# Performance work log

Measured on AMD Instinct MI355X. Metric: run time of the kernel, lower is better.

The kernel has to match this reference:

```python
import jax, jax.numpy as jnp
import numpy as np

B, N, C, H = 4, 2048, 1024, 16
D = C // H

def setup_inputs() -> dict:
    key = jax.random.key(0)
    k1, k2, k3 = jax.random.split(key, 3)
    x = jax.random.normal(k1, (B, N, C), dtype=jnp.float32)
    w_qkv = jax.random.normal(k2, (C, 3 * C), dtype=jnp.float32) * (C ** -0.5)
    w_proj = jax.random.normal(k3, (C, C), dtype=jnp.float32) * (C ** -0.5)
    b_proj = jnp.zeros((C,), dtype=jnp.float32)
    return {"x": x, "w_qkv": w_qkv, "w_proj": w_proj, "b_proj": b_proj}

def reference(x, w_qkv, w_proj, b_proj):
    scale = D ** -0.5
    qkv = x @ w_qkv                                   # [B,N,3C]
    qkv = qkv.reshape(B, N, 3, H, D).transpose(2, 0, 3, 1, 4)  # [3,B,H,N,D]
    q, k, v = qkv[0], qkv[1], qkv[2]
    attn = jnp.einsum('bhnd,bhmd->bhnm', q, k) * scale  # [B,H,N,N]
    attn = jax.nn.softmax(attn, axis=-1)
    o = jnp.einsum('bhnm,bhmd->bhnd', attn, v)          # [B,H,N,D]
    o = o.transpose(0, 2, 1, 3).reshape(B, N, C)
    return o @ w_proj + b_proj
```

## Files before the change

### kernel.cpp

```cpp
#include <hip/hip_runtime.h>
#include <hip/hip_bf16.h>


#define B_ 4
#define N_ 2048
#define C_ 1024
#define H_ 16
#define D_ 64
#define MCONST 24.0f

typedef __attribute__((ext_vector_type(8))) __bf16 bf16x8;
typedef __attribute__((ext_vector_type(4))) float f32x4;
typedef __attribute__((ext_vector_type(16))) float f32x16;
typedef unsigned int u32;
typedef __attribute__((ext_vector_type(2))) u32 u32x2;
typedef __attribute__((ext_vector_type(4))) u32 u32x4;

__device__ inline unsigned short f2bf(float f) {
  __bf16 h = (__bf16)f;
  return __builtin_bit_cast(unsigned short, h);
}

__device__ __forceinline__ u32 pk2(float lo, float hi) {
  return (u32)f2bf(lo) | ((u32)f2bf(hi) << 16);
}

__device__ __forceinline__ void gld16(const void* g, void* l) {
  __builtin_amdgcn_global_load_lds(
      (const __attribute__((address_space(1))) u32*)g,
      (__attribute__((address_space(3))) u32*)l, 16, 0, 0);
}

__global__ __launch_bounds__(256) void cvt_bf16_kernel(
    const float* __restrict__ in, unsigned short* __restrict__ out) {
  int i = (blockIdx.x * 256 + threadIdx.x) * 8;
  float4 f0 = *(const float4*)&in[i];
  float4 f1 = *(const float4*)&in[i + 4];
  ushort4 h0, h1;
  h0.x = f2bf(f0.x); h0.y = f2bf(f0.y); h0.z = f2bf(f0.z); h0.w = f2bf(f0.w);
  h1.x = f2bf(f1.x); h1.y = f2bf(f1.y); h1.z = f2bf(f1.z); h1.w = f2bf(f1.w);
  *(ushort4*)&out[i] = h0;
  *(ushort4*)&out[i + 4] = h1;
}

__global__ __launch_bounds__(256) void transpose_cvt_kernel(
    const float* __restrict__ in, unsigned short* __restrict__ out,
    int K, int Nn) {
  __shared__ float tile[32][33];
  const int t = threadIdx.x;
  const int k0 = blockIdx.y * 32, n0 = blockIdx.x * 32;
  {
    int r = t >> 3, c = (t & 7) * 4;
    float4 f = *(const float4*)&in[(size_t)(k0 + r) * Nn + n0 + c];
    tile[r][c + 0] = f.x; tile[r][c + 1] = f.y;
    tile[r][c + 2] = f.z; tile[r][c + 3] = f.w;
  }
  __syncthreads();
  {
    int nr = t >> 3, kc = (t & 7) * 4;
    ushort4 h;
    h.x = f2bf(tile[kc + 0][nr]);
    h.y = f2bf(tile[kc + 1][nr]);
    h.z = f2bf(tile[kc + 2][nr]);
    h.w = f2bf(tile[kc + 3][nr]);
    *(ushort4*)&out[(size_t)(n0 + nr) * K + k0 + kc] = h;
  }
}

__global__ __launch_bounds__(256) void transpose_v_kernel(
    const unsigned short* __restrict__ vb, unsigned short* __restrict__ vtb) {
  __shared__ u32 tile[64][65];
  const int tid = threadIdx.x;
  const int n0 = blockIdx.x * 64;
  const int bh = blockIdx.y;
  const size_t base = (size_t)bh * N_ * D_;
#pragma unroll
  for (int i = 0; i < 2; i++) {
    int id = i * 256 + tid;
    int row = id >> 3, c8 = id & 7;
    uint4 v = *(const uint4*)&vb[base + (size_t)(n0 + row) * D_ + c8 * 8];
    const unsigned short* pv = (const unsigned short*)&v;
#pragma unroll
    for (int j = 0; j < 8; j++) tile[row][c8 * 8 + j] = pv[j];
  }
  __syncthreads();
#pragma unroll
  for (int i = 0; i < 2; i++) {
    int id = i * 256 + tid;
    int d = id >> 3, nc = id & 7;
    uint4 o;
    unsigned short* po = (unsigned short*)&o;
#pragma unroll
    for (int j = 0; j < 8; j++) po[j] = (unsigned short)tile[nc * 8 + j][d];
    *(uint4*)&vtb[base + (size_t)d * N_ + n0 + nc * 8] = o;
  }
}

template<int MODE>
__global__ __launch_bounds__(256) void gemm128_kernel(
    const unsigned short* __restrict__ A, const unsigned short* __restrict__ Bt,
    const float* __restrict__ bias,
    unsigned short* __restrict__ qb, unsigned short* __restrict__ kb,
    unsigned short* __restrict__ vb, float* __restrict__ outp,
    int M, int K, int Nout)
{
  __shared__ unsigned short Al[128 * 64];
  __shared__ unsigned short Bl[128 * 64];
  const int tid = threadIdx.x;
  const int w = tid >> 6, lane = tid & 63;
  const int l15 = lane & 15, lk = lane >> 4;
  const int wr = w >> 1, wc = w & 1;
  const int n0 = blockIdx.x * 128, m0 = blockIdx.y * 128;
  const int srow = tid >> 3;
  const int scol = (tid & 7) * 8;

  f32x4 acc[4][4];
#pragma unroll
  for (int m = 0; m < 4; m++)
#pragma unroll
    for (int n = 0; n < 4; n++) acc[m][n] = f32x4{0.f, 0.f, 0.f, 0.f};

  for (int kt = 0; kt < K; kt += 64) {
#pragma unroll
    for (int i = 0; i < 4; i++)
      gld16(&A[(size_t)(m0 + i * 32 + srow) * K + kt + scol],
            &Al[i * 2048 + w * 512]);
#pragma unroll
    for (int i = 0; i < 4; i++)
      gld16(&Bt[(size_t)(n0 + i * 32 + srow) * K + kt + scol],
            &Bl[i * 2048 + w * 512]);
    __syncthreads();

#pragma unroll
    for (int kk = 0; kk < 2; kk++) {
      bf16x8 af[4], bf[4];
#pragma unroll
      for (int m = 0; m < 4; m++)
        af[m] = *(const bf16x8*)&Al[(wr * 64 + m * 16 + l15) * 64 + kk * 32 + lk * 8];
#pragma unroll
      for (int n = 0; n < 4; n++)
        bf[n] = *(const bf16x8*)&Bl[(wc * 64 + n * 16 + l15) * 64 + kk * 32 + lk * 8];
#pragma unroll
      for (int m = 0; m < 4; m++)
#pragma unroll
        for (int n = 0; n < 4; n++)
          acc[m][n] = __builtin_amdgcn_mfma_f32_16x16x32_bf16(af[m], bf[n], acc[m][n], 0, 0, 0);
    }
    __syncthreads();
  }

  if (MODE == 0) {
#pragma unroll
    for (int n = 0; n < 4; n++) {
      int c = n0 + wc * 64 + n * 16 + l15;
      int tsel = c >> 10, h = (c >> 6) & 15, d = c & 63;
      unsigned short* dst = (tsel == 0) ? qb : (tsel == 1 ? kb : vb);
      float sc = (tsel == 0) ? 0.125f * 1.44269504088896340736f : 1.0f;
#pragma unroll
      for (int m = 0; m < 4; m++) {
#pragma unroll
        for (int r = 0; r < 4; r++) {
          int row = m0 + wr * 64 + m * 16 + lk * 4 + r;
          int b = row >> 11, nn = row & 2047;
          dst[(((size_t)(b * 16 + h)) * 2048 + nn) * 64 + d] = f2bf(acc[m][n][r] * sc);
        }
      }
    }
  } else {
#pragma unroll
    for (int n = 0; n < 4; n++) {
      int c = n0 + wc * 64 + n * 16 + l15;
      float bv = bias[c];
#pragma unroll
      for (int m = 0; m < 4; m++) {
#pragma unroll
        for (int r = 0; r < 4; r++) {
          int row = m0 + wr * 64 + m * 16 + lk * 4 + r;
          outp[(size_t)row * Nout + c] = acc[m][n][r] + bv;
        }
      }
    }
  }
}

__global__ __launch_bounds__(512) void flash_kernel(
    const unsigned short* __restrict__ qb, const unsigned short* __restrict__ kb,
    const unsigned short* __restrict__ vtb, unsigned short* __restrict__ ob)
{
  __shared__ unsigned short KVs[2][2][2][64 * 64];
  __shared__ float Lf[2][128];
  float* scratch = (float*)&KVs[0][0][0][0];

  const int tid = threadIdx.x;
  const int w = tid >> 6;
  const int lane = tid & 63;
  const int l31 = lane & 31;
  const int hi = lane >> 5;
  const int g = w >> 2;
  const int ws = w & 3;
  const int q0 = blockIdx.x * 128;
  const int bh = blockIdx.y;
  const size_t base = (size_t)bh * N_ * D_;
  const unsigned short* Qg = qb + base;
  const unsigned short* Kg = kb + base;
  const unsigned short* Vtg = vtb + base;

  const int t8 = tid & 255;
  const int s_r = t8 >> 3;
  const int s_sl = (t8 & 7) ^ (s_r & 7);
  const int swz = (lane & 7) << 3;

  const int qrow_g = q0 + ws * 32 + l31;
  bf16x8 qf[4];
#pragma unroll
  for (int ds = 0; ds < 4; ds++)
    qf[ds] = *(const bf16x8*)&Qg[(size_t)qrow_g * 64 + ds * 16 + hi * 8];

  f32x16 acc0, acc1, minit;
#pragma unroll
  for (int i = 0; i < 16; i++) { acc0[i] = 0.f; acc1[i] = 0.f; minit[i] = -MCONST; }
  float lrow = 0.f;

  const int kvbeg = g * (N_ / 2);

#pragma unroll
  for (int i = 0; i < 2; i++)
    gld16(&Kg[(size_t)(kvbeg + i * 32 + s_r) * 64 + s_sl * 8],
          &KVs[g][0][0][i * 2048 + ws * 512]);
#pragma unroll
  for (int i = 0; i < 2; i++)
    gld16(&Vtg[(size_t)(i * 32 + s_r) * N_ + kvbeg + s_sl * 8],
          &KVs[g][0][1][i * 2048 + ws * 512]);

  int cur = 0;
  for (int it = 0; it < 16; ++it) {
    __syncthreads();

    if (it + 1 < 16) {
      int kvn = kvbeg + (it + 1) * 64;
#pragma unroll
      for (int i = 0; i < 2; i++)
        gld16(&Kg[(size_t)(kvn + i * 32 + s_r) * 64 + s_sl * 8],
              &KVs[g][cur ^ 1][0][i * 2048 + ws * 512]);
#pragma unroll
      for (int i = 0; i < 2; i++)
        gld16(&Vtg[(size_t)(i * 32 + s_r) * N_ + kvn + s_sl * 8],
              &KVs[g][cur ^ 1][1][i * 2048 + ws * 512]);
    }

    const unsigned short* Kl = &KVs[g][cur][0][0];
    const unsigned short* Vl = &KVs[g][cur][1][0];

    u32 F[4][4];
#pragma unroll
    for (int t = 0; t < 2; t++) {
      f32x16 sa = minit;
      __builtin_amdgcn_s_setprio(1);
#pragma unroll
      for (int ds = 0; ds < 4; ds++) {
        bf16x8 a = *(const bf16x8*)&Kl[(t * 32 + l31) * 64 + ((ds * 16 + hi * 8) ^ swz)];
        sa = __builtin_amdgcn_mfma_f32_32x32x16_bf16(a, qf[ds], sa, 0, 0, 0);
      }
      __builtin_amdgcn_s_setprio(0);

      float p[16];
#pragma unroll
      for (int r = 0; r < 16; r++) p[r] = __builtin_amdgcn_exp2f(sa[r]);
      lrow += ((p[0] + p[1]) + (p[2] + p[3])) + ((p[4] + p[5]) + (p[6] + p[7]))
            + ((p[8] + p[9]) + (p[10] + p[11])) + ((p[12] + p[13]) + (p[14] + p[15]));

      u32 pk[8];
#pragma unroll
      for (int j = 0; j < 8; j++) pk[j] = pk2(p[2 * j], p[2 * j + 1]);
#if __has_builtin(__builtin_amdgcn_permlane32_swap)
      u32x2 r02 = __builtin_amdgcn_permlane32_swap(pk[0], pk[2], false, false);
      u32x2 r13 = __builtin_amdgcn_permlane32_swap(pk[1], pk[3], false, false);
      u32x2 r46 = __builtin_amdgcn_permlane32_swap(pk[4], pk[6], false, false);
      u32x2 r57 = __builtin_amdgcn_permlane32_swap(pk[5], pk[7], false, false);
      F[2 * t][0] = r02[0]; F[2 * t][2] = r02[1];
      F[2 * t][1] = r13[0]; F[2 * t][3] = r13[1];
      F[2 * t + 1][0] = r46[0]; F[2 * t + 1][2] = r46[1];
      F[2 * t + 1][1] = r57[0]; F[2 * t + 1][3] = r57[1];
#else
      u32 sw[8];
#pragma unroll
      for (int j = 0; j < 8; j++) sw[j] = (u32)__shfl_xor((int)pk[j], 32);
      F[2 * t][0] = hi ? sw[2] : pk[0];
      F[2 * t][1] = hi ? sw[3] : pk[1];
      F[2 * t][2] = hi ? pk[2] : sw[0];
      F[2 * t][3] = hi ? pk[3] : sw[1];
      F[2 * t + 1][0] = hi ? sw[6] : pk[4];
      F[2 * t + 1][1] = hi ? sw[7] : pk[5];
      F[2 * t + 1][2] = hi ? pk[6] : sw[4];
      F[2 * t + 1][3] = hi ? pk[7] : sw[5];
#endif
    }

    __builtin_amdgcn_s_setprio(1);
#pragma unroll
    for (int ks = 0; ks < 4; ks++) {
      u32x4 fv = {F[ks][0], F[ks][1], F[ks][2], F[ks][3]};
      bf16x8 a = __builtin_bit_cast(bf16x8, fv);
      bf16x8 b0 = *(const bf16x8*)&Vl[(0 * 32 + l31) * 64 + ((ks * 16 + hi * 8) ^ swz)];
      acc0 = __builtin_amdgcn_mfma_f32_32x32x16_bf16(a, b0, acc0, 0, 0, 0);
      bf16x8 b1 = *(const bf16x8*)&Vl[(1 * 32 + l31) * 64 + ((ks * 16 + hi * 8) ^ swz)];
      acc1 = __builtin_amdgcn_mfma_f32_32x32x16_bf16(a, b1, acc1, 0, 0, 0);
    }
    __builtin_amdgcn_s_setprio(0);
    cur ^= 1;
  }

  float rs = lrow + __shfl_xor(lrow, 32);
  if (lane < 32) Lf[g][ws * 32 + l31] = rs;
  __syncthreads();

  if (g == 0) {
#pragma unroll
    for (int r = 0; r < 16; r++) {
      int qr = (r & 3) + 8 * (r >> 2) + 4 * hi;
      scratch[(ws * 32 + qr) * 64 + l31]      = acc0[r];
      scratch[(ws * 32 + qr) * 64 + 32 + l31] = acc1[r];
    }
  }
  __syncthreads();
  if (g == 1) {
    const int b = bh >> 4, h = bh & 15;
#pragma unroll
    for (int r = 0; r < 16; r++) {
      int qr = (r & 3) + 8 * (r >> 2) + 4 * hi;
      float inv = 1.0f / (Lf[0][ws * 32 + qr] + Lf[1][ws * 32 + qr]);
      float o0 = scratch[(ws * 32 + qr) * 64 + l31]      + acc0[r];
      float o1 = scratch[(ws * 32 + qr) * 64 + 32 + l31] + acc1[r];
      int nq = q0 + ws * 32 + qr;
      size_t ob0 = (((size_t)b * N_ + nq) * H_ + h) * D_;
      ob[ob0 + l31]      = f2bf(o0 * inv);
      ob[ob0 + 32 + l31] = f2bf(o1 * inv);
    }
  }
}

extern "C" void kernel_launch(void* const* d_in, const int* in_sizes, int n_in,
                              void* d_out, int out_size, void* d_ws, size_t ws_size,
                              hipStream_t stream) {
  const float* x      = (const float*)d_in[0];
  const float* w_qkv  = (const float*)d_in[1];
  const float* w_proj = (const float*)d_in[2];
  const float* b_proj = (const float*)d_in[3];
  float* out = (float*)d_out;

  const size_t qsz = (size_t)B_ * H_ * N_ * D_;
  unsigned short* qb     = (unsigned short*)d_ws;
  unsigned short* kb     = qb + qsz;
  unsigned short* vb     = kb + qsz;
  unsigned short* vtb    = vb + qsz;
  unsigned short* xbf    = vtb + qsz;
  unsigned short* ob     = xbf;
  unsigned short* wqkv_t = xbf + qsz;
  unsigned short* wproj_t= wqkv_t + (size_t)3072 * 1024;

  cvt_bf16_kernel<<<4096, 256, 0, stream>>>(x, xbf);
  transpose_cvt_kernel<<<dim3(3072 / 32, 1024 / 32), 256, 0, stream>>>(w_qkv, wqkv_t, 1024, 3072);
  transpose_cvt_kernel<<<dim3(1024 / 32, 1024 / 32), 256, 0, stream>>>(w_proj, wproj_t, 1024, 1024);

  gemm128_kernel<0><<<dim3(3072 / 128, 8192 / 128), 256, 0, stream>>>(
      xbf, wqkv_t, nullptr, qb, kb, vb, nullptr, 8192, 1024, 3072);

  transpose_v_kernel<<<dim3(N_ / 64, B_ * H_), 256, 0, stream>>>(vb, vtb);

  flash_kernel<<<dim3(N_ / 128, B_ * H_), 512, 0, stream>>>(qb, kb, vtb, ob);

  gemm128_kernel<1><<<dim3(1024 / 128, 8192 / 128), 256, 0, stream>>>(
      ob, wproj_t, b_proj, nullptr, nullptr, nullptr, out, 8192, 1024, 1024);
}
```

Measured before the change: 224.0 us.

## Add 256x256 triple-buffered QKV GEMM with async global-to-LDS loads

Replaces the 128x128 QKV projection GEMM with a 256x256 tile kernel of 512 threads. It uses a three-stage LDS ring filled by direct global-to-LDS loads, XOR-swizzled LDS columns, waitcnt-based barriers and s_setprio around the MFMA blocks. The goal is to overlap memory loads with MFMA work and raise reuse per tile. In exchange it needs many more accumulator registers and launches fewer blocks (384) on the large GPU, which can lower occupancy. The output projection keeps the old kernel, now specialised without the template.

```diff
diff --git a/kernel.cpp b/kernel.cpp
--- a/kernel.cpp
+++ b/kernel.cpp
@@ -96,12 +96,130 @@
   }
 }
 
-template<int MODE>
+__global__ __launch_bounds__(512, 1) void gemm256_kernel(
+    const unsigned short* __restrict__ A, const unsigned short* __restrict__ Bt,
+    unsigned short* __restrict__ qb, unsigned short* __restrict__ kb,
+    unsigned short* __restrict__ vb, int M, int K, int Nout)
+{
+  __shared__ unsigned short LDS[3][2][256 * 32];
+  const int tid = threadIdx.x;
+  const int w = tid >> 6, lane = tid & 63;
+  const int l15 = lane & 15, lk = lane >> 4;
+  const int wm = w >> 2, wn = w & 3;
+  const int n0 = blockIdx.x * 256, m0 = blockIdx.y * 256;
+
+  const int s_row = tid >> 2;
+  const int s_col = ((tid & 3) * 8) ^ (((s_row >> 3) & 1) * 16);
+  const int s_dst = tid * 8;
+  const int kcol = (lk * 8) ^ (((l15 >> 3) & 1) * 16);
+
+  f32x4 acc[8][4];
+#pragma unroll
+  for (int m = 0; m < 8; m++)
+#pragma unroll
+    for (int n = 0; n < 4; n++) acc[m][n] = f32x4{0.f, 0.f, 0.f, 0.f};
+
+#pragma unroll
+  for (int i = 0; i < 2; i++)
+    gld16(&A[(size_t)(m0 + i * 128 + s_row) * K + s_col],
+          &LDS[0][0][i * 4096 + s_dst]);
+#pragma unroll
+  for (int i = 0; i < 2; i++)
+    gld16(&Bt[(size_t)(n0 + i * 128 + s_row) * K + s_col],
+          &LDS[0][1][i * 4096 + s_dst]);
+
+  int cur = 0;
+  for (int j = 0; j < 31; ++j) {
+    const int nxt = (cur + 1 == 3) ? 0 : cur + 1;
+    const int kt = (j + 1) * 32;
+#pragma unroll
+    for (int i = 0; i < 2; i++)
+      gld16(&A[(size_t)(m0 + i * 128 + s_row) * K + kt + s_col],
+            &LDS[nxt][0][i * 4096 + s_dst]);
+    asm volatile("s_waitcnt vmcnt(2)" ::: "memory");
+    __builtin_amdgcn_s_barrier();
+    asm volatile("" ::: "memory");
+
+    bf16x8 bf[4], af[4];
+#pragma unroll
+    for (int n = 0; n < 4; n++)
+      bf[n] = *(const bf16x8*)&LDS[cur][1][(wn * 64 + n * 16 + l15) * 32 + kcol];
+#pragma unroll
+    for (int m = 0; m < 4; m++)
+      af[m] = *(const bf16x8*)&LDS[cur][0][(wm * 128 + m * 16 + l15) * 32 + kcol];
+    __builtin_amdgcn_s_setprio(1);
+#pragma unroll
+    for (int m = 0; m < 4; m++)
+#pragma unroll
+      for (int n = 0; n < 4; n++)
+        acc[m][n] = __builtin_amdgcn_mfma_f32_16x16x32_bf16(af[m], bf[n], acc[m][n], 0, 0, 0);
+    __builtin_amdgcn_s_setprio(0);
+
+#pragma unroll
+    for (int i = 0; i < 2; i++)
+      gld16(&Bt[(size_t)(n0 + i * 128 + s_row) * K + kt + s_col],
+            &LDS[nxt][1][i * 4096 + s_dst]);
+
+#pragma unroll
+    for (int m = 0; m < 4; m++)
+      af[m] = *(const bf16x8*)&LDS[cur][0][(wm * 128 + (m + 4) * 16 + l15) * 32 + kcol];
+    __builtin_amdgcn_s_setprio(1);
+#pragma unroll
+    for (int m = 0; m < 4; m++)
+#pragma unroll
+      for (int n = 0; n < 4; n++)
+        acc[m + 4][n] = __builtin_amdgcn_mfma_f32_16x16x32_bf16(af[m], bf[n], acc[m + 4][n], 0, 0, 0);
+    __builtin_amdgcn_s_setprio(0);
+    cur = nxt;
+  }
+
+  asm volatile("s_waitcnt vmcnt(0)" ::: "memory");
+  __builtin_amdgcn_s_barrier();
+  asm volatile("" ::: "memory");
+  {
+    bf16x8 bf[4], af[4];
+#pragma unroll
+    for (int n = 0; n < 4; n++)
+      bf[n] = *(const bf16x8*)&LDS[cur][1][(wn * 64 + n * 16 + l15) * 32 + kcol];
+#pragma unroll
+    for (int m = 0; m < 4; m++)
+      af[m] = *(const bf16x8*)&LDS[cur][0][(wm * 128 + m * 16 + l15) * 32 + kcol];
+#pragma unroll
+    for (int m = 0; m < 4; m++)
+#pragma unroll
+      for (int n = 0; n < 4; n++)
+        acc[m][n] = __builtin_amdgcn_mfma_f32_16x16x32_bf16(af[m], bf[n], acc[m][n], 0, 0, 0);
+#pragma unroll
+    for (int m = 0; m < 4; m++)
+      af[m] = *(const bf16x8*)&LDS[cur][0][(wm * 128 + (m + 4) * 16 + l15) * 32 + kcol];
+#pragma unroll
+    for (int m = 0; m < 4; m++)
+#pragma unroll
+      for (int n = 0; n < 4; n++)
+        acc[m + 4][n] = __builtin_amdgcn_mfma_f32_16x16x32_bf16(af[m], bf[n], acc[m + 4][n], 0, 0, 0);
+  }
+
+#pragma unroll
+  for (int n = 0; n < 4; n++) {
+    int c = n0 + wn * 64 + n * 16 + l15;
+    int tsel = c >> 10, h = (c >> 6) & 15, d = c & 63;
+    unsigned short* dst = (tsel == 0) ? qb : (tsel == 1 ? kb : vb);
+    float sc = (tsel == 0) ? 0.125f * 1.44269504088896340736f : 1.0f;
+#pragma unroll
+    for (int m = 0; m < 8; m++) {
+#pragma unroll
+      for (int r = 0; r < 4; r++) {
+        int row = m0 + wm * 128 + m * 16 + lk * 4 + r;
+        int b = row >> 11, nn = row & 2047;
+        dst[(((size_t)(b * 16 + h)) * 2048 + nn) * 64 + d] = f2bf(acc[m][n][r] * sc);
+      }
+    }
+  }
+}
+
 __global__ __launch_bounds__(256) void gemm128_kernel(
     const unsigned short* __restrict__ A, const unsigned short* __restrict__ Bt,
-    const float* __restrict__ bias,
-    unsigned short* __restrict__ qb, unsigned short* __restrict__ kb,
-    unsigned short* __restrict__ vb, float* __restrict__ outp,
+    const float* __restrict__ bias, float* __restrict__ outp,
     int M, int K, int Nout)
 {
   __shared__ unsigned short Al[128 * 64];
@@ -149,35 +267,16 @@
     __syncthreads();
   }
 
-  if (MODE == 0) {
-#pragma unroll
-    for (int n = 0; n < 4; n++) {
-      int c = n0 + wc * 64 + n * 16 + l15;
-      int tsel = c >> 10, h = (c >> 6) & 15, d = c & 63;
-      unsigned short* dst = (tsel == 0) ? qb : (tsel == 1 ? kb : vb);
-      float sc = (tsel == 0) ? 0.125f * 1.44269504088896340736f : 1.0f;
-#pragma unroll
-      for (int m = 0; m < 4; m++) {
-#pragma unroll
-        for (int r = 0; r < 4; r++) {
-          int row = m0 + wr * 64 + m * 16 + lk * 4 + r;
-          int b = row >> 11, nn = row & 2047;
-          dst[(((size_t)(b * 16 + h)) * 2048 + nn) * 64 + d] = f2bf(acc[m][n][r] * sc);
-        }
-      }
-    }
-  } else {
-#pragma unroll
-    for (int n = 0; n < 4; n++) {
-      int c = n0 + wc * 64 + n * 16 + l15;
-      float bv = bias[c];
-#pragma unroll
-      for (int m = 0; m < 4; m++) {
-#pragma unroll
-        for (int r = 0; r < 4; r++) {
-          int row = m0 + wr * 64 + m * 16 + lk * 4 + r;
-          outp[(size_t)row * Nout + c] = acc[m][n][r] + bv;
-        }
+#pragma unroll
+  for (int n = 0; n < 4; n++) {
+    int c = n0 + wc * 64 + n * 16 + l15;
+    float bv = bias[c];
+#pragma unroll
+    for (int m = 0; m < 4; m++) {
+#pragma unroll
+      for (int r = 0; r < 4; r++) {
+        int row = m0 + wr * 64 + m * 16 + lk * 4 + r;
+        outp[(size_t)row * Nout + c] = acc[m][n][r] + bv;
       }
     }
   }
@@ -362,13 +461,13 @@
   transpose_cvt_kernel<<<dim3(3072 / 32, 1024 / 32), 256, 0, stream>>>(w_qkv, wqkv_t, 1024, 3072);
   transpose_cvt_kernel<<<dim3(1024 / 32, 1024 / 32), 256, 0, stream>>>(w_proj, wproj_t, 1024, 1024);
 
-  gemm128_kernel<0><<<dim3(3072 / 128, 8192 / 128), 256, 0, stream>>>(
-      xbf, wqkv_t, nullptr, qb, kb, vb, nullptr, 8192, 1024, 3072);
+  gemm256_kernel<<<dim3(3072 / 256, 8192 / 256), 512, 0, stream>>>(
+      xbf, wqkv_t, qb, kb, vb, 8192, 1024, 3072);
 
   transpose_v_kernel<<<dim3(N_ / 64, B_ * H_), 256, 0, stream>>>(vb, vtb);
 
   flash_kernel<<<dim3(N_ / 128, B_ * H_), 512, 0, stream>>>(qb, kb, vtb, ob);
 
-  gemm128_kernel<1><<<dim3(1024 / 128, 8192 / 128), 256, 0, stream>>>(
-      ob, wproj_t, b_proj, nullptr, nullptr, nullptr, out, 8192, 1024, 1024);
-}
+  gemm128_kernel<<<dim3(1024 / 128, 8192 / 128), 256, 0, stream>>>(
+      ob, wproj_t, b_proj, out, 8192, 1024, 1024);
+}
```

Result: faster. 217.4 us (-3.0%).
